# Kernel tuning notes

Hardware: AMD Instinct MI355X
Metric: run time of the kernel (lower is better)

The kernel has to match this reference:

```python
import jax, jax.numpy as jnp
import numpy as np

DIM = 384; HEADS = 16; HEAD_DIM = DIM // HEADS; HID = 4 * DIM
ETA_SCALE = 0.01; CLIP_INNER = 1.0; EPS = 1e-5
B = 8; T_FR = 32; GH = 16; GW = 16; CHUNK = 8; N = T_FR * GH * GW
D_SEG = 2 * (HEAD_DIM // 3 // 2)  # 8 dims each for t/h/w rotation (3*8 == head_dim)


def _layernorm(x, g, b):
    m = jnp.mean(x, -1, keepdims=True)
    v = jnp.var(x, -1, keepdims=True)
    return (x - m) * jax.lax.rsqrt(v + EPS) * g + b


def _mlp(W1, b1, W2, b2, x):
    # 2-layer Titan memory / CMS level MLP: dim -> 4*dim -> dim, GELU
    return jax.nn.gelu(x @ W1 + b1) @ W2 + b2


def _rope_seg(x, pos):
    # x: [..., s] interleaved-pair RoPE with positions pos (broadcastable to x[..., 0])
    s = x.shape[-1]; half = s // 2
    freqs = 1.0 / (10000.0 ** (jnp.arange(half, dtype=x.dtype) / half))
    ang = pos[..., None] * freqs
    c, si = jnp.cos(ang), jnp.sin(ang)
    x1, x2 = x[..., 0::2], x[..., 1::2]
    return jnp.stack([x1 * c - x2 * si, x1 * si + x2 * c], -1).reshape(x.shape)


def _apply_rope(x, tp, hp, wp):
    # 3D RoPE per head over (t, h, w) position segments
    b, n, d = x.shape
    xh = x.reshape(b, n, HEADS, HEAD_DIM)
    s = D_SEG
    parts = [_rope_seg(xh[..., 0:s], tp[None, :, None]),
             _rope_seg(xh[..., s:2 * s], hp[None, :, None]),
             _rope_seg(xh[..., 2 * s:3 * s], wp[None, :, None])]
    if 3 * s < HEAD_DIM:
        parts.append(xh[..., 3 * s:])
    return jnp.concatenate(parts, -1).reshape(b, n, d)


def _forward(x, norm1_g, norm1_b, q_W, tW1, tb1, tW2, tb2, out_W, out_b,
             norm2_g, norm2_b, cms_W1, cms_b1, cms_W2, cms_b2, T, H, W, chunk_size):
    Bx, Nt, D = x.shape
    y = _layernorm(x, norm1_g, norm1_b)
    nc = T // chunk_size
    Cper = chunk_size * H * W
    y_ch = y.reshape(Bx, nc, Cper, D).swapaxes(0, 1)  # [nc, B, Cper, D]
    # per-chunk RoPE positions (positions restart each chunk, matching _titan_forward_chunk)
    tp = jnp.repeat(jnp.arange(chunk_size, dtype=x.dtype), H * W)
    hp = jnp.tile(jnp.repeat(jnp.arange(H, dtype=x.dtype), W), chunk_size)
    wp = jnp.tile(jnp.arange(W, dtype=x.dtype), chunk_size * H)

    def mem_loss(W1, b1, W2, b2, kk, tt):
        return jnp.mean((_mlp(W1, b1, W2, b2, kk) - tt) ** 2)

    grad_fn = jax.grad(mem_loss, argnums=(0, 1, 2, 3))
    mlp_v = jax.vmap(_mlp, in_axes=(0, 0, 0, 0, None))

    def step(carry, yc):
        W1s, b1s, W2s, b2s = carry  # stacked [5, ...]: k, v, eta, alpha, memory
        gen = mlp_v(W1s[:4], b1s[:4], W2s[:4], b2s[:4], yc)  # [4, B, C, D]
        k, v, eta_raw, alpha_raw = gen[0], gen[1], gen[2], gen[3]
        eta = jax.nn.softplus(eta_raw) * ETA_SCALE
        alpha = jax.nn.sigmoid(alpha_raw)
        q = yc @ q_W
        q = _apply_rope(q, tp, hp, wp)
        k = _apply_rope(k, tp, hp, wp)
        out = _mlp(W1s[4], b1s[4], W2s[4], b2s[4], q)  # retrieve from main memory
        # surprise signal (per-token retrieval error norm); threshold=0 -> always update
        # surprise = jnp.linalg.norm(v - out, axis=-1)
        # self-targets v_hat = M_box(v) for the 4 adaptive memories; main memory targets v
        vhat = mlp_v(W1s[:4], b1s[:4], W2s[:4], b2s[:4], v)
        targets = jnp.concatenate([jax.lax.stop_gradient(vhat), v[None]], 0)  # [5,B,C,D]
        g1, g2, g3, g4 = jax.vmap(grad_fn, in_axes=(0, 0, 0, 0, None, 0))(
            W1s, b1s, W2s, b2s, k, targets)
        norm = jnp.sqrt(jnp.sum(g1 * g1, (1, 2)) + jnp.sum(g2 * g2, 1)
                        + jnp.sum(g3 * g3, (1, 2)) + jnp.sum(g4 * g4, 1))
        sc = jnp.minimum(1.0, CLIP_INNER / (norm + 1e-12))  # inner grad clip per memory
        em = jnp.mean(eta); am = jnp.mean(alpha)
        # DGD update with decay alpha and lr eta: p <- (1-alpha)*p - eta*g
        W1n = (1 - am) * W1s - em * g1 * sc[:, None, None]
        b1n = (1 - am) * b1s - em * g2 * sc[:, None]
        W2n = (1 - am) * W2s - em * g3 * sc[:, None, None]
        b2n = (1 - am) * b2s - em * g4 * sc[:, None]
        return (W1n, b1n, W2n, b2n), out

    _, outs = jax.lax.scan(step, (tW1, tb1, tW2, tb2), y_ch)
    titan = outs.swapaxes(0, 1).reshape(Bx, Nt, D) @ out_W + out_b
    x2 = x + titan
    # Phase B: CMS multi-frequency MLP cascade (sequential chain of level MLPs)
    h = _layernorm(x2, norm2_g, norm2_b)
    for l in range(cms_W1.shape[0]):
        h = _mlp(cms_W1[l], cms_b1[l], cms_W2[l], cms_b2[l], h)
    return x2 + h


def setup_inputs() -> dict:
    key = jax.random.key(0)
    ks = jax.random.split(key, 8)
    s = 0.02
    f = jnp.float32
    return {
        'x': jax.random.normal(ks[0], (B, N, DIM), f),
        'norm1_g': jnp.ones((DIM,), f), 'norm1_b': jnp.zeros((DIM,), f),
        'q_W': jax.random.normal(ks[1], (DIM, DIM), f) * s,
        'tW1': jax.random.normal(ks[2], (5, DIM, HID), f) * s,
        'tb1': jnp.zeros((5, HID), f),
        'tW2': jax.random.normal(ks[3], (5, HID, DIM), f) * s,
        'tb2': jnp.zeros((5, DIM), f),
        'out_W': jax.random.normal(ks[4], (DIM, DIM), f) * s,
        'out_b': jnp.zeros((DIM,), f),
        'norm2_g': jnp.ones((DIM,), f), 'norm2_b': jnp.zeros((DIM,), f),
        'cms_W1': jax.random.normal(ks[5], (3, DIM, HID), f) * s,
        'cms_b1': jnp.zeros((3, HID), f),
        'cms_W2': jax.random.normal(ks[6], (3, HID, DIM), f) * s,
        'cms_b2': jnp.zeros((3, DIM), f),
        'T': T_FR, 'H': GH, 'W': GW, 'chunk_size': CHUNK,
    }


def reference(x, norm1_g, norm1_b, q_W, tW1, tb1, tW2, tb2, out_W, out_b,
              norm2_g, norm2_b, cms_W1, cms_b1, cms_W2, cms_b2, T, H, W, chunk_size):
    return _forward(x, norm1_g, norm1_b, q_W, tW1, tb1, tW2, tb2, out_W, out_b,
                    norm2_g, norm2_b, cms_W1, cms_b1, cms_W2, cms_b2, T, H, W, chunk_size)
```

## Files before the change

kernel.cpp:

```cpp
#include <hip/hip_runtime.h>
#include <cstddef>
#include <cstdint>


typedef __bf16 bf16;
typedef __bf16 bf16x4 __attribute__((ext_vector_type(4)));
typedef __bf16 bf16x8 __attribute__((ext_vector_type(8)));
typedef float  f32x4  __attribute__((ext_vector_type(4)));

constexpr float INV_CNT = 1.0f / 6291456.0f;

__device__ __forceinline__ float fast_gelu(float x) {
  float u = 0.7978845608028654f * (x + 0.044715f * x * x * x);
  return x / (1.0f + __expf(-2.0f * u));
}
__device__ __forceinline__ float fast_gelu_grad(float x) {
  float x2 = x * x;
  float u = 0.7978845608028654f * (x + 0.044715f * x * x2);
  float s = 1.0f / (1.0f + __expf(-2.0f * u));
  return s + x * s * (1.0f - s) * 1.5957691216057308f * (1.0f + 0.134145f * x2);
}
__device__ __forceinline__ f32x4 gelu4(f32x4 v) {
  v[0] = fast_gelu(v[0]); v[1] = fast_gelu(v[1]);
  v[2] = fast_gelu(v[2]); v[3] = fast_gelu(v[3]);
  return v;
}
__device__ __forceinline__ bf16x4 tobf4(f32x4 v) {
  bf16x4 o; o[0] = (bf16)v[0]; o[1] = (bf16)v[1]; o[2] = (bf16)v[2]; o[3] = (bf16)v[3];
  return o;
}
__device__ __forceinline__ f32x4 tof4(bf16x4 v) {
  return f32x4{(float)v[0], (float)v[1], (float)v[2], (float)v[3]};
}

__device__ __forceinline__ void gload16(const bf16* g, void* lds) {
  __builtin_amdgcn_global_load_lds(
      (const __attribute__((address_space(1))) void*)g,
      (__attribute__((address_space(3))) void*)lds, 16, 0, 0);
}

template <int N>
__device__ __forceinline__ void wait_vmcnt() {
  if constexpr (N == 0)      asm volatile("s_waitcnt vmcnt(0)" ::: "memory");
  else if constexpr (N == 4) asm volatile("s_waitcnt vmcnt(4)" ::: "memory");
  else if constexpr (N == 6) asm volatile("s_waitcnt vmcnt(6)" ::: "memory");
  __builtin_amdgcn_sched_barrier(0);
}

__device__ __forceinline__ int xcd_chunk(int id, int n) {
  int q = n >> 3, r = n & 7;
  int xcd = id & 7, pos = id >> 3;
  return (xcd < r ? xcd * (q + 1) : r * (q + 1) + (xcd - r) * q) + pos;
}

__global__ __launch_bounds__(64)
void ln_kernel(const float* __restrict__ x, const float* __restrict__ g,
               const float* __restrict__ b, bf16* __restrict__ y,
               int shift, int base, int stride) {
  int r = blockIdx.x;
  int src = ((r >> shift) * stride) + base + (r & ((1 << shift) - 1));
  int lane = threadIdx.x;
  const float* xr = x + (size_t)src * 384;
  float vals[6];
  float s = 0.f, s2 = 0.f;
#pragma unroll
  for (int i = 0; i < 6; ++i) {
    float v = xr[lane + i * 64];
    vals[i] = v; s += v; s2 += v * v;
  }
#pragma unroll
  for (int o = 32; o > 0; o >>= 1) { s += __shfl_xor(s, o); s2 += __shfl_xor(s2, o); }
  float m = s * (1.0f / 384.0f);
  float var = s2 * (1.0f / 384.0f) - m * m;
  float rr = rsqrtf(var + 1e-5f);
  bf16* yr = y + (size_t)r * 384;
#pragma unroll
  for (int i = 0; i < 6; ++i) {
    int c = lane + i * 64;
    yr[c] = (bf16)((vals[i] - m) * rr * g[c] + b[c]);
  }
}

__device__ __forceinline__ void trw_body(const float* in, bf16* out, int R, int C,
                                         int c0, int r0, int tid) {
  __shared__ float t[32][33];
  int tr = tid >> 3, tc = (tid & 7) * 4;
  f32x4 v = *(const f32x4*)&in[(size_t)(r0 + tr) * C + c0 + tc];
  t[tr][tc + 0] = v[0]; t[tr][tc + 1] = v[1]; t[tr][tc + 2] = v[2]; t[tr][tc + 3] = v[3];
  __syncthreads();
  bf16x4 o;
  o[0] = (bf16)t[tc + 0][tr]; o[1] = (bf16)t[tc + 1][tr];
  o[2] = (bf16)t[tc + 2][tr]; o[3] = (bf16)t[tc + 3][tr];
  *(bf16x4*)&out[(size_t)(c0 + tr) * R + r0 + tc] = o;
}

__global__ __launch_bounds__(256)
void trans_state(const float* __restrict__ SW1, const float* __restrict__ SW2,
                 bf16* __restrict__ sw1t, bf16* __restrict__ sw2t) {
  int z = blockIdx.z;
  if (z < 5)
    trw_body(SW1 + (size_t)z * 589824, sw1t + (size_t)z * 589824, 384, 1536,
             blockIdx.x * 32, blockIdx.y * 32, threadIdx.x);
  else
    trw_body(SW2 + (size_t)(z - 5) * 589824, sw2t + (size_t)(z - 5) * 589824, 1536, 384,
             blockIdx.y * 32, blockIdx.x * 32, threadIdx.x);
}

__global__ __launch_bounds__(256)
void trans_static(const float* __restrict__ qW, const float* __restrict__ outW,
                  const float* __restrict__ cW1, const float* __restrict__ cW2,
                  bf16* __restrict__ qwt, bf16* __restrict__ owt,
                  bf16* __restrict__ cw1t, bf16* __restrict__ cw2t) {
  int z = blockIdx.z;
  if (z < 2) {
    if (blockIdx.x >= 12) return;
    trw_body(z ? outW : qW, z ? owt : qwt, 384, 384,
             blockIdx.x * 32, blockIdx.y * 32, threadIdx.x);
  } else if (z < 5) {
    int lc = z - 2;
    trw_body(cW1 + (size_t)lc * 589824, cw1t + (size_t)lc * 589824, 384, 1536,
             blockIdx.x * 32, blockIdx.y * 32, threadIdx.x);
  } else {
    int lc = z - 5;
    trw_body(cW2 + (size_t)lc * 589824, cw2t + (size_t)lc * 589824, 1536, 384,
             blockIdx.y * 32, blockIdx.x * 32, threadIdx.x);
  }
}

__global__ __launch_bounds__(256)
void tr_bf(const bf16* __restrict__ in, bf16* __restrict__ out, int R, int C) {
  __shared__ bf16 t[32][36];
  int r0 = blockIdx.x * 32, c0 = blockIdx.y * 32;
  int tr = threadIdx.x >> 3, tc = (threadIdx.x & 7) * 4;
  bf16x4 v = *(const bf16x4*)&in[(size_t)(r0 + tr) * C + c0 + tc];
  t[tr][tc + 0] = v[0]; t[tr][tc + 1] = v[1]; t[tr][tc + 2] = v[2]; t[tr][tc + 3] = v[3];
  __syncthreads();
  bf16x4 o;
  o[0] = t[tc + 0][tr]; o[1] = t[tc + 1][tr]; o[2] = t[tc + 2][tr]; o[3] = t[tc + 3][tr];
  *(bf16x4*)&out[(size_t)(c0 + tr) * R + r0 + tc] = o;
}

__global__ __launch_bounds__(256)
void copy_bf16(const float* __restrict__ in, bf16* __restrict__ out, int n) {
  int i = (blockIdx.x * 256 + threadIdx.x) * 4;
  if (i < n) {
    f32x4 v = *(const f32x4*)&in[i];
    *(bf16x4*)&out[i] = tobf4(v);
  }
}

enum { E_BF16 = 0, E_GELU, E_PAIR, E_SUB, E_MUL, E_F32ADD, E_KV, E_RED2 };

template <int EPI, int BM>
__global__ __launch_bounds__(BM == 128 ? 512 : 256)
void mm_fwd(const bf16* __restrict__ Act, int lda, const bf16* __restrict__ W,
            const float* __restrict__ bias, const bf16* __restrict__ baux,
            const float* __restrict__ faux, float* __restrict__ red,
            bf16* __restrict__ Cb, bf16* __restrict__ C2, bf16* __restrict__ Ct,
            float* __restrict__ Cf, int K, int ldc, int ldt, float scale,
            int croff, int cshift, int cbase, int cstride,
            long zA, long zW, int zB) {
  constexpr int NW = (BM == 128) ? 8 : 4;
  constexpr int NFM = 2;
  constexpr int TW = 16 / NW;
  constexpr int TA = (BM / 8) / NW;
  constexpr int LPT = TW + TA;
  constexpr int SWE = 128 * 64;
  constexpr int SAE = BM * 64;
  constexpr bool TRANS = (EPI == E_PAIR || EPI == E_SUB || EPI == E_MUL);
  __shared__ bf16 smem[2 * SWE + 2 * SAE];
  const int z = blockIdx.z;
  Act += (size_t)z * zA;
  W   += (size_t)z * zW;
  if (bias) bias += (size_t)z * zB;
  const int nx = gridDim.x;
  const int nid = xcd_chunk(blockIdx.y * nx + blockIdx.x, nx * gridDim.y);
  const int m0 = (nid / nx) * BM, i0 = (nid % nx) * 128;
  const int tid = threadIdx.x;
  const int l = tid & 63, w = tid >> 6;
  const int a = l & 15, g = l >> 4;
  const int wi0 = (w & 1) * 64, wm0 = (w >> 1) * 32;
  const int lrow = l >> 3;
  const int lcolel = (((l & 7) ^ lrow) << 4) >> 1;

  const bf16* wp = W   + (size_t)(i0 + lrow) * K   + lcolel;
  const bf16* ap = Act + (size_t)(m0 + lrow) * lda + lcolel;

  f32x4 acc[4][NFM];
#pragma unroll
  for (int i = 0; i < 4; ++i)
#pragma unroll
    for (int j = 0; j < NFM; ++j) acc[i][j] = f32x4{0.f, 0.f, 0.f, 0.f};

  auto stage = [&](int buf, int k0) {
    bf16* dW = smem + buf * SWE;
    bf16* dA = smem + 2 * SWE + buf * SAE;
#pragma unroll
    for (int t = 0; t < TW; ++t) {
      const int seg = w * TW + t;
      gload16(wp + (size_t)(seg * 8) * K + k0, (char*)dW + seg * 1024);
    }
#pragma unroll
    for (int t = 0; t < TA; ++t) {
      const int seg = w * TA + t;
      gload16(ap + (size_t)(seg * 8) * lda + k0, (char*)dA + seg * 1024);
    }
  };

  const int nIt = K >> 6;
  stage(0, 0);
  for (int it = 0; it < nIt; ++it) {
    const int cur = it & 1;
    if (it + 1 < nIt) { stage(cur ^ 1, (it + 1) << 6); wait_vmcnt<LPT>(); }
    else              { wait_vmcnt<0>(); }
    __builtin_amdgcn_s_barrier();
    const bf16* bW = smem + cur * SWE;
    const bf16* bA = smem + 2 * SWE + cur * SAE;
#pragma unroll
    for (int kh = 0; kh < 2; ++kh) {
      bf16x8 Af[4], Bf[NFM];
#pragma unroll
      for (int f = 0; f < 4; ++f) {
        const int rW = wi0 + f * 16 + a;
        Af[f] = *(const bf16x8*)((const char*)bW +
                 ((rW * 128 + kh * 64 + g * 16) ^ ((rW & 7) << 4)));
      }
#pragma unroll
      for (int f = 0; f < NFM; ++f) {
        const int rA = wm0 + f * 16 + a;
        Bf[f] = *(const bf16x8*)((const char*)bA +
                 ((rA * 128 + kh * 64 + g * 16) ^ ((rA & 7) << 4)));
      }
#pragma unroll
      for (int fi = 0; fi < 4; ++fi)
#pragma unroll
        for (int fm = 0; fm < NFM; ++fm)
          acc[fi][fm] = __builtin_amdgcn_mfma_f32_16x16x32_bf16(Af[fi], Bf[fm], acc[fi][fm], 0, 0, 0);
    }
    asm volatile("s_waitcnt lgkmcnt(0)" ::: "memory");
    __builtin_amdgcn_s_barrier();
  }

  if constexpr (EPI == E_RED2) {
    float ssum = 0.f;
#pragma unroll
    for (int fi = 0; fi < 4; ++fi) {
      f32x4 b4 = *(const f32x4*)&bias[i0 + wi0 + fi * 16 + g * 4];
#pragma unroll
      for (int fm = 0; fm < NFM; ++fm)
#pragma unroll
        for (int r = 0; r < 4; ++r) {
          float vv = acc[fi][fm][r] + b4[r];
          if (z == 0) ssum += fmaxf(vv, 0.f) + log1pf(__expf(-fabsf(vv)));
          else        ssum += 1.0f / (1.0f + __expf(-vv));
        }
    }
#pragma unroll
    for (int o = 32; o > 0; o >>= 1) ssum += __shfl_xor(ssum, o);
    float* wred = (float*)smem;
    if (l == 0) wred[w] = ssum;
    __syncthreads();
    if (tid == 0) {
      float t2 = 0.f;
      for (int q = 0; q < NW; ++q) t2 += wred[q];
      atomicAdd(&red[z], t2);
    }
    return;
  } else {
    float* T = (float*)smem + w * (16 * 68);
    const int iB = i0 + wi0;
    f32x4 b4 = f32x4{0.f, 0.f, 0.f, 0.f};
    if (bias) b4 = *(const f32x4*)&bias[iB + a * 4];
#pragma unroll
    for (int fm = 0; fm < NFM; ++fm) {
#pragma unroll
      for (int fi = 0; fi < 4; ++fi)
        *(f32x4*)&T[a * 68 + fi * 16 + g * 4] = acc[fi][fm];
      asm volatile("s_waitcnt lgkmcnt(0)" ::: "memory");
      __builtin_amdgcn_sched_barrier(0);

#pragma unroll
      for (int q = 0; q < 4; ++q) {
        const int ml = wm0 + fm * 16 + q * 4 + g;
        const int trow = q * 4 + g;
        f32x4 v = *(const f32x4*)&T[trow * 68 + a * 4];
        v += b4;
        if constexpr (EPI == E_F32ADD) {
          const int rr = croff + m0 + ml;
          const int crow = ((rr >> cshift) * cstride) + cbase + (rr & ((1 << cshift) - 1));
          const size_t cb = (size_t)crow * ldc + iB + a * 4;
          v += *(const f32x4*)&faux[cb];
          *(f32x4*)&Cf[cb] = v;
        } else {
          const size_t cb = (size_t)(m0 + ml) * ldc + iB + a * 4;
          if constexpr (EPI == E_BF16) {
            *(bf16x4*)&Cb[cb] = tobf4(v);
          } else if constexpr (EPI == E_KV) {
            bf16* DST = (z == 0) ? Cb : C2;
            *(bf16x4*)&DST[cb] = tobf4(v);
          } else if constexpr (EPI == E_GELU) {
            *(bf16x4*)&Cb[cb] = tobf4(gelu4(v));
          } else if constexpr (EPI == E_PAIR) {
            *(bf16x4*)&Cb[cb] = tobf4(v);
            f32x4 gv = gelu4(v);
            *(bf16x4*)&C2[cb] = tobf4(gv);
            *(f32x4*)&T[trow * 68 + a * 4] = gv;
          } else if constexpr (EPI == E_SUB) {
            f32x4 t4 = tof4(*(const bf16x4*)&baux[cb]);
            v = (v - t4) * scale;
            *(bf16x4*)&Cb[cb] = tobf4(v);
            *(f32x4*)&T[trow * 68 + a * 4] = v;
          } else if constexpr (EPI == E_MUL) {
            f32x4 h4 = tof4(*(const bf16x4*)&baux[cb]);
            v[0] *= fast_gelu_grad(h4[0]); v[1] *= fast_gelu_grad(h4[1]);
            v[2] *= fast_gelu_grad(h4[2]); v[3] *= fast_gelu_grad(h4[3]);
            *(f32x4*)&T[trow * 68 + a * 4] = v;
          }
        }
      }

      if constexpr (TRANS) {
        asm volatile("s_waitcnt lgkmcnt(0)" ::: "memory");
        __builtin_amdgcn_sched_barrier(0);
        const int mg = m0 + wm0 + fm * 16;
        bf16x8 o0, o1;
#pragma unroll
        for (int j = 0; j < 16; ++j) {
          float vv = T[j * 68 + l];
          if (j < 8) o0[j] = (bf16)vv; else o1[j - 8] = (bf16)vv;
        }
        *(bf16x8*)&Ct[(size_t)(iB + l) * ldt + mg] = o0;
        *(bf16x8*)&Ct[(size_t)(iB + l) * ldt + mg + 8] = o1;
      }
    }
  }
}

__global__ __launch_bounds__(512)
void mm_tn2c(const bf16* __restrict__ P1, int ldP1, const bf16* __restrict__ Q1, int ldQ1,
             float* __restrict__ Ga, int ldGa,
             const bf16* __restrict__ P2, int ldP2, const bf16* __restrict__ Q2, int ldQ2,
             float* __restrict__ Gb, int ldGb, int mlen) {
  constexpr int SBE = 128 * 64;
  __shared__ bf16 smem[4 * SBE];
  const int nid = xcd_chunk(blockIdx.x, gridDim.x);
  const int grp = nid / 36, pair = nid % 36;
  const int part = grp & 1, zsl = grp >> 1;
  const bf16* P; const bf16* Q; float* G;
  int ldP, ldQ, ldG, p0, q0;
  if (part == 0) {
    P = P1; Q = Q1; G = Ga; ldP = ldP1; ldQ = ldQ1; ldG = ldGa;
    p0 = (pair / 3) * 128; q0 = (pair % 3) * 128;
  } else {
    P = P2; Q = Q2; G = Gb; ldP = ldP2; ldQ = ldQ2; ldG = ldGb;
    p0 = (pair / 12) * 128; q0 = (pair % 12) * 128;
  }
  const int tid = threadIdx.x;
  const int mb = zsl * mlen;
  const int l = tid & 63, w = tid >> 6;
  const int a = l & 15, g = l >> 4;
  const int wp0 = (w & 1) * 64, wq0 = (w >> 1) * 32;
  const int lrow = l >> 3;
  const int lcolel = (((l & 7) ^ lrow) << 4) >> 1;

  const bf16* pp = P + (size_t)(p0 + lrow) * ldP + lcolel;
  const bf16* qp = Q + (size_t)(q0 + lrow) * ldQ + lcolel;

  f32x4 acc[4][2];
#pragma unroll
  for (int i = 0; i < 4; ++i)
#pragma unroll
    for (int j = 0; j < 2; ++j) acc[i][j] = f32x4{0.f, 0.f, 0.f, 0.f};

  auto stage = [&](int buf, int m0) {
    bf16* dP = smem + buf * SBE;
    bf16* dQ = smem + 2 * SBE + buf * SBE;
#pragma unroll
    for (int t = 0; t < 2; ++t) {
      const int seg = w * 2 + t;
      gload16(pp + (size_t)(seg * 8) * ldP + m0, (char*)dP + seg * 1024);
      gload16(qp + (size_t)(seg * 8) * ldQ + m0, (char*)dQ + seg * 1024);
    }
  };

  const int nIt = mlen >> 6;
  stage(0, mb);
  for (int it = 0; it < nIt; ++it) {
    const int cur = it & 1;
    if (it + 1 < nIt) { stage(cur ^ 1, mb + ((it + 1) << 6)); wait_vmcnt<4>(); }
    else              { wait_vmcnt<0>(); }
    __builtin_amdgcn_s_barrier();
    const bf16* bP = smem + cur * SBE;
    const bf16* bQ = smem + 2 * SBE + cur * SBE;
#pragma unroll
    for (int kh = 0; kh < 2; ++kh) {
      bf16x8 Pf[4], Qf[2];
#pragma unroll
      for (int f = 0; f < 4; ++f) {
        const int rP = wp0 + f * 16 + a;
        Pf[f] = *(const bf16x8*)((const char*)bP +
                 ((rP * 128 + kh * 64 + g * 16) ^ ((rP & 7) << 4)));
      }
#pragma unroll
      for (int f = 0; f < 2; ++f) {
        const int rQ = wq0 + f * 16 + a;
        Qf[f] = *(const bf16x8*)((const char*)bQ +
                 ((rQ * 128 + kh * 64 + g * 16) ^ ((rQ & 7) << 4)));
      }
#pragma unroll
      for (int f1 = 0; f1 < 4; ++f1)
#pragma unroll
        for (int f2 = 0; f2 < 2; ++f2)
          acc[f1][f2] = __builtin_amdgcn_mfma_f32_16x16x32_bf16(Pf[f1], Qf[f2], acc[f1][f2], 0, 0, 0);
    }
    asm volatile("s_waitcnt lgkmcnt(0)" ::: "memory");
    __builtin_amdgcn_s_barrier();
  }
#pragma unroll
  for (int f1 = 0; f1 < 4; ++f1)
#pragma unroll
    for (int f2 = 0; f2 < 2; ++f2)
#pragma unroll
      for (int r = 0; r < 4; ++r)
        atomicAdd(&G[(size_t)(p0 + wp0 + f1 * 16 + g * 4 + r) * ldG + q0 + wq0 + f2 * 16 + a],
                  acc[f1][f2][r]);
}

__global__ __launch_bounds__(256)
void rope_kernel(bf16* __restrict__ p0, int rbase) {
  int idx = blockIdx.x * blockDim.x + threadIdx.x;
  int row = idx >> 4, hd = idx & 15;
  int j = (rbase + row) & 2047;
  float pos[3] = { (float)(j >> 8), (float)((j >> 4) & 15), (float)(j & 15) };
  const float freqs[4] = { 1.0f, 0.1f, 0.01f, 0.001f };
  bf16* p = p0 + (size_t)row * 384 + hd * 24;
#pragma unroll
  for (int s = 0; s < 3; ++s) {
    bf16x8 vv = *(bf16x8*)(p + s * 8);
#pragma unroll
    for (int pr = 0; pr < 4; ++pr) {
      float ang = pos[s] * freqs[pr];
      float si, co;
      sincosf(ang, &si, &co);
      float e0 = (float)vv[2 * pr], e1 = (float)vv[2 * pr + 1];
      vv[2 * pr]     = (bf16)(e0 * co - e1 * si);
      vv[2 * pr + 1] = (bf16)(e0 * si + e1 * co);
    }
    *(bf16x8*)(p + s * 8) = vv;
  }
}

__global__ __launch_bounds__(256)
void rowsum2(const bf16* __restrict__ ODt, const bf16* __restrict__ DAt,
             float* __restrict__ G4, float* __restrict__ G2, int mlen) {
  int r = blockIdx.x;
  const bf16* p; float* o;
  if (r < 384) { p = ODt + (size_t)r * mlen; o = G4 + r; }
  else         { p = DAt + (size_t)(r - 384) * mlen; o = G2 + (r - 384); }
  float s = 0.f;
  for (int i = threadIdx.x * 8; i < mlen; i += 256 * 8) {
    bf16x8 v = *(const bf16x8*)&p[i];
#pragma unroll
    for (int e = 0; e < 8; ++e) s += (float)v[e];
  }
  __shared__ float sm[256];
  sm[threadIdx.x] = s; __syncthreads();
  for (int o2 = 128; o2 > 0; o2 >>= 1) {
    if (threadIdx.x < o2) sm[threadIdx.x] += sm[threadIdx.x + o2];
    __syncthreads();
  }
  if (threadIdx.x == 0) atomicAdd(o, sm[0]);
}

__global__ __launch_bounds__(256)
void sumsq_all(const float* __restrict__ G1, const float* __restrict__ G2,
               const float* __restrict__ G3, const float* __restrict__ G4,
               float* __restrict__ red) {
  int i = blockIdx.y, bx = blockIdx.x;
  const float* base; int per, lb, nb;
  if (bx < 256)      { base = G1 + (size_t)i * 589824; per = 589824; lb = bx;       nb = 256; }
  else if (bx < 512) { base = G3 + (size_t)i * 589824; per = 589824; lb = bx - 256; nb = 256; }
  else if (bx < 514) { base = G2 + (size_t)i * 1536;   per = 1536;   lb = bx - 512; nb = 2; }
  else               { base = G4 + (size_t)i * 384;    per = 384;    lb = bx - 514; nb = 2; }
  float s = 0.f;
  for (int idx = lb * 256 + threadIdx.x; idx < per; idx += nb * 256) {
    float v = base[idx]; s += v * v;
  }
  __shared__ float sm[256];
  sm[threadIdx.x] = s; __syncthreads();
  for (int o = 128; o > 0; o >>= 1) {
    if (threadIdx.x < o) sm[threadIdx.x] += sm[threadIdx.x + o];
    __syncthreads();
  }
  if (threadIdx.x == 0) atomicAdd(&red[2 + i], sm[0]);
}

__global__ __launch_bounds__(256)
void update_all(float* __restrict__ SW1, float* __restrict__ SB1,
                float* __restrict__ SW2, float* __restrict__ SB2,
                const float* __restrict__ G1, const float* __restrict__ G2,
                const float* __restrict__ G3, const float* __restrict__ G4,
                const float* __restrict__ red) {
  int i = blockIdx.y, bx = blockIdx.x;
  float* S; const float* G; int per, lb, nb;
  if (bx < 512)       { S = SW1; G = G1; per = 589824; lb = bx;        nb = 512; }
  else if (bx < 1024) { S = SW2; G = G3; per = 589824; lb = bx - 512;  nb = 512; }
  else if (bx < 1028) { S = SB1; G = G2; per = 1536;   lb = bx - 1024; nb = 4; }
  else                { S = SB2; G = G4; per = 384;    lb = bx - 1028; nb = 4; }
  size_t base = (size_t)i * per;
  float em = 0.01f * red[0] * INV_CNT;
  float am = red[1] * INV_CNT;
  float norm = sqrtf(red[2 + i]);
  float sc = fminf(1.0f, 1.0f / (norm + 1e-12f));
  float ws_ = 1.0f - am;
  float gs = em * sc;
  for (int idx = lb * 256 + (int)threadIdx.x; idx < per; idx += nb * 256)
    S[base + idx] = ws_ * S[base + idx] - gs * G[base + idx];
}

extern "C" void kernel_launch(void* const* d_in, const int* in_sizes, int n_in,
                              void* d_out, int out_size, void* d_ws, size_t ws_size,
                              hipStream_t stream) {
  const float* x    = (const float*)d_in[0];
  const float* n1g  = (const float*)d_in[1];
  const float* n1b  = (const float*)d_in[2];
  const float* qW   = (const float*)d_in[3];
  const float* tW1  = (const float*)d_in[4];
  const float* tb1  = (const float*)d_in[5];
  const float* tW2  = (const float*)d_in[6];
  const float* tb2  = (const float*)d_in[7];
  const float* outW = (const float*)d_in[8];
  const float* outb = (const float*)d_in[9];
  const float* n2g  = (const float*)d_in[10];
  const float* n2b  = (const float*)d_in[11];
  const float* cW1  = (const float*)d_in[12];
  const float* cb1  = (const float*)d_in[13];
  const float* cW2  = (const float*)d_in[14];
  const float* cb2  = (const float*)d_in[15];
  float* out = (float*)d_out;

  const size_t W1SZ = 384 * 1536, W2SZ = 1536 * 384;
  const size_t STATE = 5 * W1SZ + 5 * 1536 + 5 * W2SZ + 5 * 384;
  const size_t BF_W = 21 * W1SZ + 2 * 147456;
  const size_t CHUNK_BF = 4 * (size_t)16384 * 384;
  const size_t FIXEDF = 2 * STATE + 16 + BF_W / 2 + CHUNK_BF / 2;
  size_t MS = 16384;
  while (MS > 2048 && (FIXEDF + MS * 3840) * 4 > ws_size) MS >>= 1;
  if ((FIXEDF + MS * 3840) * 4 > ws_size) {
    hipMemcpyAsync(d_out, d_in[0], (size_t)25165824 * 4, hipMemcpyDeviceToDevice, stream);
    return;
  }
  const int NS = (int)(16384 / MS);
  const int iMS = (int)MS;

  float* ws = (float*)d_ws;
  size_t off = 0;
  auto alloc = [&](size_t n) { float* p = ws + off; off += n; return p; };
  auto balloc = [&](size_t n) { bf16* p = (bf16*)(ws + off); off += (n + 1) / 2; return p; };
  float* SW1 = alloc(5 * W1SZ);
  float* SB1 = alloc(5 * 1536);
  float* SW2 = alloc(5 * W2SZ);
  float* SB2 = alloc(5 * 384);
  float* G1  = alloc(5 * W1SZ);
  float* G2  = alloc(5 * 1536);
  float* G3  = alloc(5 * W2SZ);
  float* G4  = alloc(5 * 384);
  float* RED = alloc(16);
  bf16* Yc   = balloc((size_t)16384 * 384);
  bf16* Kb   = balloc((size_t)16384 * 384);
  bf16* Vb   = balloc((size_t)16384 * 384);
  bf16* Kbt  = balloc((size_t)16384 * 384);
  bf16* sw1t = balloc(5 * W1SZ);
  bf16* sw2t = balloc(5 * W2SZ);
  bf16* sw2c = balloc(5 * W2SZ);
  bf16* qwt  = balloc(147456);
  bf16* owt  = balloc(147456);
  bf16* cw1t = balloc(3 * W1SZ);
  bf16* cw2t = balloc(3 * W2SZ);
  bf16* pool = balloc(MS * 3072);
  bf16* GH1t = balloc(MS * 1536);
  bf16* DAt  = balloc(MS * 1536);
  bf16* OD   = balloc(MS * 384);
  bf16* ODt  = balloc(MS * 384);
  bf16* T2   = balloc(MS * 384);
  bf16* Tt   = balloc(MS * 384);
  bf16* H1r  = pool;
  bf16* GH1k = pool + MS * 1536;

  hipMemcpyAsync(SW1, tW1, 5 * W1SZ * 4, hipMemcpyDeviceToDevice, stream);
  hipMemcpyAsync(SB1, tb1, 5 * 1536 * 4, hipMemcpyDeviceToDevice, stream);
  hipMemcpyAsync(SW2, tW2, 5 * W2SZ * 4, hipMemcpyDeviceToDevice, stream);
  hipMemcpyAsync(SB2, tb2, 5 * 384 * 4, hipMemcpyDeviceToDevice, stream);

  trans_static<<<dim3(48, 12, 8), 256, 0, stream>>>(qW, outW, cW1, cW2, qwt, owt, cw1t, cw2t);

  const size_t grads_bytes = STATE * 4;
  const int gm  = iMS / 128;
  const int gm2 = iMS / 64;
  int mlen_t = iMS / 8; if (mlen_t < 128) mlen_t = 128;
  if (mlen_t > 2048) mlen_t = 2048;
  const int nzt = iMS / mlen_t;
  const int tn_grid = 36 * 2 * nzt;
  const float SC = 2.0f * INV_CNT;
  const size_t MSR = (size_t)iMS * 384;

  for (int c = 0; c < 4; ++c) {
    hipMemsetAsync(G1, 0, grads_bytes, stream);
    hipMemsetAsync(RED, 0, 64, stream);
    trans_state<<<dim3(48, 12, 10), 256, 0, stream>>>(SW1, SW2, sw1t, sw2t);
    copy_bf16<<<dim3(2880), 256, 0, stream>>>(SW2, sw2c, (int)(5 * W2SZ));

    ln_kernel<<<dim3(16384), dim3(64), 0, stream>>>(x, n1g, n1b, Yc, 11, c * 2048, 8192);

    for (int s = 0; s < NS; ++s) {
      const bf16* Ys = Yc + (size_t)s * MSR;
      mm_fwd<E_GELU, 128><<<dim3(24, gm), 512, 0, stream>>>(Ys, 384, sw1t,
          SB1, nullptr, nullptr, nullptr, pool, nullptr, nullptr, nullptr,
          384, 3072, 0, 0.f, 0, 30, 0, 0, 0, 0, 0);
      mm_fwd<E_KV, 64><<<dim3(3, gm2, 2), 256, 0, stream>>>(pool, 3072, sw2t,
          SB2, nullptr, nullptr, nullptr, Kb + s * MSR, Vb + s * MSR, nullptr, nullptr,
          1536, 384, 0, 0.f, 0, 30, 0, 0, 1536, (long)W2SZ, 384);
      mm_fwd<E_GELU, 128><<<dim3(24, gm), 512, 0, stream>>>(Ys, 384, sw1t + 2 * W1SZ,
          SB1 + 2 * 1536, nullptr, nullptr, nullptr, pool, nullptr, nullptr, nullptr,
          384, 3072, 0, 0.f, 0, 30, 0, 0, 0, 0, 0);
      mm_fwd<E_RED2, 64><<<dim3(3, gm2, 2), 256, 0, stream>>>(pool, 3072, sw2t + 2 * W2SZ,
          SB2 + 2 * 384, nullptr, nullptr, RED, nullptr, nullptr, nullptr, nullptr,
          1536, 384, 0, 0.f, 0, 30, 0, 0, 1536, (long)W2SZ, 384);
    }

    for (int s = 0; s < NS; ++s) {
      const bf16* Ys = Yc + (size_t)s * MSR;
      mm_fwd<E_BF16, 64><<<dim3(3, gm2), 256, 0, stream>>>(Ys, 384, qwt,
          nullptr, nullptr, nullptr, nullptr, Tt, nullptr, nullptr, nullptr,
          384, 384, 0, 0.f, 0, 30, 0, 0, 0, 0, 0);
      rope_kernel<<<dim3(iMS / 16), 256, 0, stream>>>(Tt, s * iMS);
      mm_fwd<E_GELU, 128><<<dim3(12, gm), 512, 0, stream>>>(Tt, 384, sw1t + 4 * W1SZ,
          SB1 + 4 * 1536, nullptr, nullptr, nullptr, GH1k, nullptr, nullptr, nullptr,
          384, 1536, 0, 0.f, 0, 30, 0, 0, 0, 0, 0);
      mm_fwd<E_BF16, 64><<<dim3(3, gm2), 256, 0, stream>>>(GH1k, 1536, sw2t + 4 * W2SZ,
          SB2 + 4 * 384, nullptr, nullptr, nullptr, T2, nullptr, nullptr, nullptr,
          1536, 384, 0, 0.f, 0, 30, 0, 0, 0, 0, 0);
      mm_fwd<E_F32ADD, 64><<<dim3(3, gm2), 256, 0, stream>>>(T2, 384, owt, outb,
          nullptr, x, nullptr, nullptr, nullptr, nullptr, out,
          384, 384, 0, 0.f, s * iMS, 11, c * 2048, 8192, 0, 0, 0);
    }

    rope_kernel<<<dim3(1024), 256, 0, stream>>>(Kb, 0);
    tr_bf<<<dim3(512, 12), 256, 0, stream>>>(Kb, Kbt, 16384, 384);

    for (int s = 0; s < NS; ++s) {
      const bf16* Ks = Kb + (size_t)s * MSR;
      const bf16* Vs = Vb + (size_t)s * MSR;
      for (int i = 0; i < 5; ++i) {
        if (i < 4) {
          mm_fwd<E_GELU, 128><<<dim3(12, gm), 512, 0, stream>>>(Vs, 384, sw1t + i * W1SZ,
              SB1 + i * 1536, nullptr, nullptr, nullptr, GH1k, nullptr, nullptr, nullptr,
              384, 1536, 0, 0.f, 0, 30, 0, 0, 0, 0, 0);
          mm_fwd<E_BF16, 64><<<dim3(3, gm2), 256, 0, stream>>>(GH1k, 1536, sw2t + i * W2SZ,
              SB2 + i * 384, nullptr, nullptr, nullptr, Tt, nullptr, nullptr, nullptr,
              1536, 384, 0, 0.f, 0, 30, 0, 0, 0, 0, 0);
        }
        const bf16* tg = (i < 4) ? Tt : Vs;
        mm_fwd<E_PAIR, 128><<<dim3(12, gm), 512, 0, stream>>>(Ks, 384, sw1t + i * W1SZ,
            SB1 + i * 1536, nullptr, nullptr, nullptr, H1r, GH1k, GH1t, nullptr,
            384, 1536, iMS, 0.f, 0, 30, 0, 0, 0, 0, 0);
        mm_fwd<E_SUB, 64><<<dim3(3, gm2), 256, 0, stream>>>(GH1k, 1536, sw2t + i * W2SZ,
            SB2 + i * 384, tg, nullptr, nullptr, OD, nullptr, ODt, nullptr,
            1536, 384, iMS, SC, 0, 30, 0, 0, 0, 0, 0);
        mm_fwd<E_MUL, 128><<<dim3(12, gm), 512, 0, stream>>>(OD, 384, sw2c + i * W2SZ,
            nullptr, H1r, nullptr, nullptr, nullptr, nullptr, DAt, nullptr,
            384, 1536, iMS, 0.f, 0, 30, 0, 0, 0, 0, 0);
        mm_tn2c<<<dim3(tn_grid), 512, 0, stream>>>(
            GH1t, iMS, ODt, iMS, G3 + i * W2SZ, 384,
            Kbt + (size_t)s * iMS, 16384, DAt, iMS, G1 + i * W1SZ, 1536, mlen_t);
        rowsum2<<<dim3(1920), 256, 0, stream>>>(ODt, DAt, G4 + i * 384, G2 + i * 1536, iMS);
      }
    }

    sumsq_all<<<dim3(516, 5), 256, 0, stream>>>(G1, G2, G3, G4, RED);
    update_all<<<dim3(1032, 5), 256, 0, stream>>>(SW1, SB1, SW2, SB2, G1, G2, G3, G4, RED);
  }

  const int NCS = (int)(65536 / MS);
  for (int s2 = 0; s2 < NCS; ++s2) {
    float* outp = out + (size_t)s2 * MSR;
    ln_kernel<<<dim3(iMS), dim3(64), 0, stream>>>(out, n2g, n2b, OD, 30, s2 * iMS, 0);
    bf16* hc = OD; bf16* hn = T2;
    for (int lc = 0; lc < 3; ++lc) {
      mm_fwd<E_GELU, 128><<<dim3(12, gm), 512, 0, stream>>>(hc, 384, cw1t + lc * W1SZ,
          cb1 + lc * 1536, nullptr, nullptr, nullptr, GH1k, nullptr, nullptr, nullptr,
          384, 1536, 0, 0.f, 0, 30, 0, 0, 0, 0, 0);
      if (lc < 2) {
        mm_fwd<E_BF16, 64><<<dim3(3, gm2), 256, 0, stream>>>(GH1k, 1536, cw2t + lc * W2SZ,
            cb2 + lc * 384, nullptr, nullptr, nullptr, hn, nullptr, nullptr, nullptr,
            1536, 384, 0, 0.f, 0, 30, 0, 0, 0, 0, 0);
        bf16* t = hc; hc = hn; hn = t;
      } else {
        mm_fwd<E_F32ADD, 64><<<dim3(3, gm2), 256, 0, stream>>>(GH1k, 1536, cw2t + lc * W2SZ,
            cb2 + lc * 384, nullptr, outp, nullptr, nullptr, nullptr, nullptr, outp,
            1536, 384, 0, 0.f, 0, 30, 0, 0, 0, 0, 0);
      }
    }
  }
}
```

Measured before the change: 10.14 ms.

## Halve GEMM K-tile to 32 and fuse bias-gradient row sums into mm_tn2c

The forward GEMM kernel moves from a 64-wide to a 32-wide K step, with a new LDS swizzle and an enlarged shared buffer sized for the epilogue slab. This shrinks shared memory per block, which may allow higher occupancy, but doubles the number of barrier iterations. Separately, the rowsum2 kernel that reduced ODt/DAt for the bias gradients is removed. Blocks of mm_tn2c with p0==0 now sum the Q tiles already staged in LDS and atomically add the results, saving one launch and a full re-read of those buffers.

```diff
diff --git a/kernel.cpp b/kernel.cpp
--- a/kernel.cpp
+++ b/kernel.cpp
@@ -42,8 +42,9 @@
 template <int N>
 __device__ __forceinline__ void wait_vmcnt() {
   if constexpr (N == 0)      asm volatile("s_waitcnt vmcnt(0)" ::: "memory");
+  else if constexpr (N == 2) asm volatile("s_waitcnt vmcnt(2)" ::: "memory");
+  else if constexpr (N == 3) asm volatile("s_waitcnt vmcnt(3)" ::: "memory");
   else if constexpr (N == 4) asm volatile("s_waitcnt vmcnt(4)" ::: "memory");
-  else if constexpr (N == 6) asm volatile("s_waitcnt vmcnt(6)" ::: "memory");
   __builtin_amdgcn_sched_barrier(0);
 }
 
@@ -162,13 +163,16 @@
             long zA, long zW, int zB) {
   constexpr int NW = (BM == 128) ? 8 : 4;
   constexpr int NFM = 2;
-  constexpr int TW = 16 / NW;
-  constexpr int TA = (BM / 8) / NW;
+  constexpr int TW = 8 / NW;
+  constexpr int TA = (BM / 16) / NW;
   constexpr int LPT = TW + TA;
-  constexpr int SWE = 128 * 64;
-  constexpr int SAE = BM * 64;
+  constexpr int SWE = 128 * 32;
+  constexpr int SAE = BM * 32;
+  constexpr int BUFE = 2 * (SWE + SAE);
+  constexpr int SLABE = NW * 16 * 68 * 2;
+  constexpr int SMEME = (BUFE > SLABE) ? BUFE : SLABE;
   constexpr bool TRANS = (EPI == E_PAIR || EPI == E_SUB || EPI == E_MUL);
-  __shared__ bf16 smem[2 * SWE + 2 * SAE];
+  __shared__ bf16 smem[SMEME];
   const int z = blockIdx.z;
   Act += (size_t)z * zA;
   W   += (size_t)z * zW;
@@ -180,11 +184,12 @@
   const int l = tid & 63, w = tid >> 6;
   const int a = l & 15, g = l >> 4;
   const int wi0 = (w & 1) * 64, wm0 = (w >> 1) * 32;
-  const int lrow = l >> 3;
-  const int lcolel = (((l & 7) ^ lrow) << 4) >> 1;
-
-  const bf16* wp = W   + (size_t)(i0 + lrow) * K   + lcolel;
-  const bf16* ap = Act + (size_t)(m0 + lrow) * lda + lcolel;
+  const int srow = l >> 2;
+  const int sue = ((l & 3) ^ ((l >> 3) & 3)) * 8;
+  const int fru = (g ^ ((a >> 1) & 3)) << 4;
+
+  const bf16* wp = W   + (size_t)(i0 + srow) * K   + sue;
+  const bf16* ap = Act + (size_t)(m0 + srow) * lda + sue;
 
   f32x4 acc[4][NFM];
 #pragma unroll
@@ -198,38 +203,35 @@
 #pragma unroll
     for (int t = 0; t < TW; ++t) {
       const int seg = w * TW + t;
-      gload16(wp + (size_t)(seg * 8) * K + k0, (char*)dW + seg * 1024);
+      gload16(wp + (size_t)(seg * 16) * K + k0, (char*)dW + seg * 1024);
     }
 #pragma unroll
     for (int t = 0; t < TA; ++t) {
       const int seg = w * TA + t;
-      gload16(ap + (size_t)(seg * 8) * lda + k0, (char*)dA + seg * 1024);
+      gload16(ap + (size_t)(seg * 16) * lda + k0, (char*)dA + seg * 1024);
     }
   };
 
-  const int nIt = K >> 6;
+  const int nIt = K >> 5;
   stage(0, 0);
   for (int it = 0; it < nIt; ++it) {
     const int cur = it & 1;
-    if (it + 1 < nIt) { stage(cur ^ 1, (it + 1) << 6); wait_vmcnt<LPT>(); }
+    if (it + 1 < nIt) { stage(cur ^ 1, (it + 1) << 5); wait_vmcnt<LPT>(); }
     else              { wait_vmcnt<0>(); }
     __builtin_amdgcn_s_barrier();
     const bf16* bW = smem + cur * SWE;
     const bf16* bA = smem + 2 * SWE + cur * SAE;
-#pragma unroll
-    for (int kh = 0; kh < 2; ++kh) {
+    {
       bf16x8 Af[4], Bf[NFM];
 #pragma unroll
       for (int f = 0; f < 4; ++f) {
         const int rW = wi0 + f * 16 + a;
-        Af[f] = *(const bf16x8*)((const char*)bW +
-                 ((rW * 128 + kh * 64 + g * 16) ^ ((rW & 7) << 4)));
+        Af[f] = *(const bf16x8*)((const char*)bW + rW * 64 + fru);
       }
 #pragma unroll
       for (int f = 0; f < NFM; ++f) {
         const int rA = wm0 + f * 16 + a;
-        Bf[f] = *(const bf16x8*)((const char*)bA +
-                 ((rA * 128 + kh * 64 + g * 16) ^ ((rA & 7) << 4)));
+        Bf[f] = *(const bf16x8*)((const char*)bA + rA * 64 + fru);
       }
 #pragma unroll
       for (int fi = 0; fi < 4; ++fi)
@@ -340,21 +342,23 @@
 void mm_tn2c(const bf16* __restrict__ P1, int ldP1, const bf16* __restrict__ Q1, int ldQ1,
              float* __restrict__ Ga, int ldGa,
              const bf16* __restrict__ P2, int ldP2, const bf16* __restrict__ Q2, int ldQ2,
-             float* __restrict__ Gb, int ldGb, int mlen) {
+             float* __restrict__ Gb, int ldGb, int mlen,
+             float* __restrict__ G4s, float* __restrict__ G2s) {
   constexpr int SBE = 128 * 64;
   __shared__ bf16 smem[4 * SBE];
   const int nid = xcd_chunk(blockIdx.x, gridDim.x);
   const int grp = nid / 36, pair = nid % 36;
   const int part = grp & 1, zsl = grp >> 1;
-  const bf16* P; const bf16* Q; float* G;
+  const bf16* P; const bf16* Q; float* G; float* Gsum;
   int ldP, ldQ, ldG, p0, q0;
   if (part == 0) {
-    P = P1; Q = Q1; G = Ga; ldP = ldP1; ldQ = ldQ1; ldG = ldGa;
+    P = P1; Q = Q1; G = Ga; ldP = ldP1; ldQ = ldQ1; ldG = ldGa; Gsum = G4s;
     p0 = (pair / 3) * 128; q0 = (pair % 3) * 128;
   } else {
-    P = P2; Q = Q2; G = Gb; ldP = ldP2; ldQ = ldQ2; ldG = ldGb;
+    P = P2; Q = Q2; G = Gb; ldP = ldP2; ldQ = ldQ2; ldG = ldGb; Gsum = G2s;
     p0 = (pair / 12) * 128; q0 = (pair % 12) * 128;
   }
+  const bool doSum = (p0 == 0);
   const int tid = threadIdx.x;
   const int mb = zsl * mlen;
   const int l = tid & 63, w = tid >> 6;
@@ -371,6 +375,10 @@
   for (int i = 0; i < 4; ++i)
 #pragma unroll
     for (int j = 0; j < 2; ++j) acc[i][j] = f32x4{0.f, 0.f, 0.f, 0.f};
+  float qsum = 0.f;
+  const int srow = w * 16 + (l & 15);
+  const int u0 = ((l >> 4) ^ (l & 7)) & 7;
+  const int u1 = u0 ^ 4;
 
   auto stage = [&](int buf, int m0) {
     bf16* dP = smem + buf * SBE;
@@ -413,6 +421,12 @@
         for (int f2 = 0; f2 < 2; ++f2)
           acc[f1][f2] = __builtin_amdgcn_mfma_f32_16x16x32_bf16(Pf[f1], Qf[f2], acc[f1][f2], 0, 0, 0);
     }
+    if (doSum) {
+      bf16x8 s0 = *(const bf16x8*)((const char*)bQ + srow * 128 + u0 * 16);
+      bf16x8 s1 = *(const bf16x8*)((const char*)bQ + srow * 128 + u1 * 16);
+#pragma unroll
+      for (int e = 0; e < 8; ++e) qsum += (float)s0[e] + (float)s1[e];
+    }
     asm volatile("s_waitcnt lgkmcnt(0)" ::: "memory");
     __builtin_amdgcn_s_barrier();
   }
@@ -424,6 +438,11 @@
       for (int r = 0; r < 4; ++r)
         atomicAdd(&G[(size_t)(p0 + wp0 + f1 * 16 + g * 4 + r) * ldG + q0 + wq0 + f2 * 16 + a],
                   acc[f1][f2][r]);
+  if (doSum) {
+    qsum += __shfl_xor(qsum, 16);
+    qsum += __shfl_xor(qsum, 32);
+    if (l < 16) atomicAdd(&Gsum[q0 + w * 16 + l], qsum);
+  }
 }
 
 __global__ __launch_bounds__(256)
@@ -448,28 +467,6 @@
     }
     *(bf16x8*)(p + s * 8) = vv;
   }
-}
-
-__global__ __launch_bounds__(256)
-void rowsum2(const bf16* __restrict__ ODt, const bf16* __restrict__ DAt,
-             float* __restrict__ G4, float* __restrict__ G2, int mlen) {
-  int r = blockIdx.x;
-  const bf16* p; float* o;
-  if (r < 384) { p = ODt + (size_t)r * mlen; o = G4 + r; }
-  else         { p = DAt + (size_t)(r - 384) * mlen; o = G2 + (r - 384); }
-  float s = 0.f;
-  for (int i = threadIdx.x * 8; i < mlen; i += 256 * 8) {
-    bf16x8 v = *(const bf16x8*)&p[i];
-#pragma unroll
-    for (int e = 0; e < 8; ++e) s += (float)v[e];
-  }
-  __shared__ float sm[256];
-  sm[threadIdx.x] = s; __syncthreads();
-  for (int o2 = 128; o2 > 0; o2 >>= 1) {
-    if (threadIdx.x < o2) sm[threadIdx.x] += sm[threadIdx.x + o2];
-    __syncthreads();
-  }
-  if (threadIdx.x == 0) atomicAdd(o, sm[0]);
 }
 
 __global__ __launch_bounds__(256)
@@ -672,8 +669,8 @@
             384, 1536, iMS, 0.f, 0, 30, 0, 0, 0, 0, 0);
         mm_tn2c<<<dim3(tn_grid), 512, 0, stream>>>(
             GH1t, iMS, ODt, iMS, G3 + i * W2SZ, 384,
-            Kbt + (size_t)s * iMS, 16384, DAt, iMS, G1 + i * W1SZ, 1536, mlen_t);
-        rowsum2<<<dim3(1920), 256, 0, stream>>>(ODt, DAt, G4 + i * 384, G2 + i * 1536, iMS);
+            Kbt + (size_t)s * iMS, 16384, DAt, iMS, G1 + i * W1SZ, 1536, mlen_t,
+            G4 + i * 384, G2 + i * 1536);
       }
     }
 
```

After: 9.250 ms. 1.1x faster.
